# Optimization experiments

Measured on AMD Instinct MI355X. Metric: run time of the kernel, lower is better.

## Reference

```python
import jax, jax.numpy as jnp
import numpy as np

B, L, D, H = 4, 1024, 768, 12
HD = D // H  # head_dim = 64
SCALING = HD ** -0.5


def setup_inputs() -> dict:
    key = jax.random.key(0)
    ks = jax.random.split(key, 6)
    x = jax.random.normal(ks[0], (B, L, D), dtype=jnp.float32)
    attn_bias = jax.random.normal(ks[1], (B, H, L, L), dtype=jnp.float32)
    s_in = 1.0 / np.sqrt(D)
    w_in = jax.random.uniform(ks[2], (3 * D, D), dtype=jnp.float32, minval=-s_in, maxval=s_in)
    b_in = jax.random.uniform(ks[3], (3 * D,), dtype=jnp.float32, minval=-s_in, maxval=s_in)
    w_out = jax.random.uniform(ks[4], (D, D), dtype=jnp.float32, minval=-s_in, maxval=s_in)
    b_out = jax.random.uniform(ks[5], (D,), dtype=jnp.float32, minval=-s_in, maxval=s_in)
    return {"x": x, "attn_bias": attn_bias, "w_in": w_in, "b_in": b_in,
            "w_out": w_out, "b_out": b_out}


def reference(x, attn_bias, w_in, b_in, w_out, b_out):
    # fused QKV projection: [B, L, 3D]
    qkv = jnp.einsum('bld,ed->ble', x, w_in) + b_in
    q, k, v = jnp.split(qkv, 3, axis=-1)
    # [B, H, L, HD]
    q = q.reshape(B, L, H, HD).transpose(0, 2, 1, 3) * SCALING
    k = k.reshape(B, L, H, HD).transpose(0, 2, 1, 3)
    v = v.reshape(B, L, H, HD).transpose(0, 2, 1, 3)
    # bias-augmented attention scores: [B, H, L, L]
    scores = jnp.einsum('bhqd,bhkd->bhqk', q, k) + attn_bias
    probs = jax.nn.softmax(scores, axis=-1)
    # attend: [B, H, L, HD] -> [B, L, D]
    o = jnp.einsum('bhqk,bhkd->bhqd', probs, v)
    o = o.transpose(0, 2, 1, 3).reshape(B, L, D)
    return jnp.einsum('bld,ed->ble', o, w_out) + b_out
```

## Files before the change

kernel.cpp:

```cpp
#include <hip/hip_runtime.h>
#include <hip/hip_bf16.h>
#include <stdint.h>

#define B_ 4
#define L_ 1024
#define D_ 768
#define H_ 12
#define HD_ 64
#define M_ 4096
#define N3_ 2304

typedef float f32x4 __attribute__((ext_vector_type(4)));
typedef float f32x4v __attribute__((ext_vector_type(4)));
typedef short bf16x8 __attribute__((ext_vector_type(8)));
typedef unsigned short u16;
typedef u16 u16x8 __attribute__((ext_vector_type(8)));
typedef u16 u16x4 __attribute__((ext_vector_type(4)));

#define AS3 __attribute__((address_space(3)))
#define AS1 __attribute__((address_space(1)))

__device__ __forceinline__ void gll16(const void* g, void* l) {
  __builtin_amdgcn_global_load_lds((const AS1 void*)g, (AS3 void*)l, 16, 0, 0);
}

__device__ __forceinline__ u16 f2bf(float f) {
  uint32_t u = __builtin_bit_cast(uint32_t, f);
  u += 0x7fffu + ((u >> 16) & 1u);
  return (u16)(u >> 16);
}

__global__ void k_cvt(const float* __restrict__ in, u16* __restrict__ out, int n4) {
  int i = blockIdx.x * 256 + threadIdx.x;
  if (i < n4) {
    f32x4v v = ((const f32x4v*)in)[i];
    u16x4 o;
    o.x = f2bf(v.x); o.y = f2bf(v.y); o.z = f2bf(v.z); o.w = f2bf(v.w);
    ((u16x4*)out)[i] = o;
  }
}

__global__ __launch_bounds__(256) void k_gemm_qkv(
    const u16* __restrict__ Xb, const u16* __restrict__ Wb,
    const float* __restrict__ b_in,
    u16* __restrict__ gQ, u16* __restrict__ gK, u16* __restrict__ gV) {
  __shared__ u16 As[128 * 64];
  __shared__ u16 Bs[128 * 64];
  const int tid = threadIdx.x;
  const int lane = tid & 63;
  const int w = tid >> 6;
  const int wm = (w >> 1) * 64;
  const int wn = (w & 1) * 64;
  const int lr = lane & 15;
  const int lg = lane >> 4;
  const int m0 = blockIdx.x * 128;
  const int n0 = blockIdx.y * 128;

  f32x4 acc[4][4];
#pragma unroll
  for (int i = 0; i < 4; ++i)
#pragma unroll
    for (int j = 0; j < 4; ++j) acc[i][j] = (f32x4){0.f, 0.f, 0.f, 0.f};

  for (int kt = 0; kt < 12; ++kt) {
    __syncthreads();
#pragma unroll
    for (int i = 0; i < 4; ++i) {
      int seg = i * 256 + tid;
      int row = seg >> 3;
      int sl = (seg & 7) ^ (row & 7);
      gll16(Xb + (size_t)(m0 + row) * 768 + kt * 64 + sl * 8, (char*)As + seg * 16);
      gll16(Wb + (size_t)(n0 + row) * 768 + kt * 64 + sl * 8, (char*)Bs + seg * 16);
    }
    __syncthreads();
#pragma unroll
    for (int kh = 0; kh < 2; ++kh) {
      bf16x8 af[4], bfr[4];
#pragma unroll
      for (int t = 0; t < 4; ++t) {
        int ra = wm + t * 16 + lr;
        af[t] = *(const bf16x8*)((const char*)As + ra * 128 +
                                 ((kh * 64 + lg * 16) ^ ((ra & 7) << 4)));
        int rb = wn + t * 16 + lr;
        bfr[t] = *(const bf16x8*)((const char*)Bs + rb * 128 +
                                  ((kh * 64 + lg * 16) ^ ((rb & 7) << 4)));
      }
#pragma unroll
      for (int mi = 0; mi < 4; ++mi)
#pragma unroll
        for (int ni = 0; ni < 4; ++ni)
          acc[mi][ni] = __builtin_amdgcn_mfma_f32_16x16x32_bf16(
              af[mi], bfr[ni], acc[mi][ni], 0, 0, 0);
    }
  }
  const int sec = blockIdx.y / 6;
  u16* dst = sec == 0 ? gQ : (sec == 1 ? gK : gV);
  const float scale = sec == 0 ? 0.125f : 1.0f;
#pragma unroll
  for (int ni = 0; ni < 4; ++ni) {
    int e = n0 + wn + ni * 16 + lr;
    float bias = b_in[e];
    int es = e - sec * 768;
    int h = es >> 6, d = es & 63;
#pragma unroll
    for (int mi = 0; mi < 4; ++mi) {
#pragma unroll
      for (int j = 0; j < 4; ++j) {
        int m = m0 + wm + mi * 16 + lg * 4 + j;
        int bb = m >> 10, lq = m & 1023;
        float vv = (acc[mi][ni][j] + bias) * scale;
        dst[(size_t)((bb * 12 + h) * 1024 + lq) * 64 + d] = f2bf(vv);
      }
    }
  }
}

__global__ __launch_bounds__(256) void k_transpose(const u16* __restrict__ V,
                                                   u16* __restrict__ Vt) {
  __shared__ u16 t[64][66];
  const int tid = threadIdx.x;
  const int bh = blockIdx.x >> 4;
  const int kv0 = (blockIdx.x & 15) * 64;
  {
    int r = tid >> 2, c0 = (tid & 3) * 16;
    const u16* src = V + (size_t)(bh * 1024 + kv0 + r) * 64 + c0;
#pragma unroll
    for (int p = 0; p < 2; ++p) {
      u16x8 x = *(const u16x8*)(src + p * 8);
#pragma unroll
      for (int e = 0; e < 8; ++e) t[r][c0 + p * 8 + e] = x[e];
    }
  }
  __syncthreads();
  {
    int d = tid >> 2, k0 = (tid & 3) * 16;
    u16* dst = Vt + (size_t)(bh * 64 + d) * 1024 + kv0 + k0;
#pragma unroll
    for (int p = 0; p < 2; ++p) {
      u16x8 o;
#pragma unroll
      for (int e = 0; e < 8; ++e) o[e] = t[k0 + p * 8 + e][d];
      *(u16x8*)(dst + p * 8) = o;
    }
  }
}

__global__ __launch_bounds__(256) void k_attn(
    const u16* __restrict__ gQ, const u16* __restrict__ gK,
    const u16* __restrict__ gVt, const float* __restrict__ gBias,
    u16* __restrict__ gO) {
  __shared__ u16 Ks[64 * 64];
  __shared__ u16 Vs[64 * 64];
  __shared__ u16 Pl[4][16 * 64];
  const int tid = threadIdx.x;
  const int lane = tid & 63;
  const int w = tid >> 6;
  const int lr = lane & 15;
  const int lg = lane >> 4;
  const int bh = blockIdx.x >> 4;
  const int q0 = (blockIdx.x & 15) * 64;
  const int qr = q0 + w * 16;

  bf16x8 qa[2];
#pragma unroll
  for (int kh = 0; kh < 2; ++kh)
    qa[kh] = *(const bf16x8*)(gQ + (size_t)(bh * 1024 + qr + lr) * 64 + kh * 32 + lg * 8);

  f32x4 oacc[4];
#pragma unroll
  for (int dt = 0; dt < 4; ++dt) oacc[dt] = (f32x4){0.f, 0.f, 0.f, 0.f};
  float mrow[4] = {-1e30f, -1e30f, -1e30f, -1e30f};
  float lrow[4] = {0.f, 0.f, 0.f, 0.f};

  for (int kv0 = 0; kv0 < 1024; kv0 += 64) {
    __syncthreads();
#pragma unroll
    for (int i = 0; i < 2; ++i) {
      int seg = i * 256 + tid;
      int row = seg >> 3;
      int sl = (seg & 7) ^ (row & 7);
      gll16(gK + (size_t)(bh * 1024 + kv0 + row) * 64 + sl * 8, (char*)Ks + seg * 16);
      gll16(gVt + (size_t)(bh * 64 + row) * 1024 + kv0 + sl * 8, (char*)Vs + seg * 16);
    }
    __syncthreads();

    f32x4 s[4];
#pragma unroll
    for (int ni = 0; ni < 4; ++ni) s[ni] = (f32x4){0.f, 0.f, 0.f, 0.f};
#pragma unroll
    for (int kh = 0; kh < 2; ++kh) {
#pragma unroll
      for (int ni = 0; ni < 4; ++ni) {
        int rb = ni * 16 + lr;
        bf16x8 kb = *(const bf16x8*)((const char*)Ks + rb * 128 +
                                     ((kh * 64 + lg * 16) ^ ((rb & 7) << 4)));
        s[ni] = __builtin_amdgcn_mfma_f32_16x16x32_bf16(qa[kh], kb, s[ni], 0, 0, 0);
      }
    }
    const float* bp = gBias + (size_t)(bh * 1024 + qr) * 1024 + kv0;
#pragma unroll
    for (int ni = 0; ni < 4; ++ni)
#pragma unroll
      for (int j = 0; j < 4; ++j)
        s[ni][j] += bp[(size_t)(lg * 4 + j) * 1024 + ni * 16 + lr];

#pragma unroll
    for (int j = 0; j < 4; ++j) {
      float vm = fmaxf(fmaxf(s[0][j], s[1][j]), fmaxf(s[2][j], s[3][j]));
      vm = fmaxf(vm, __shfl_xor(vm, 1));
      vm = fmaxf(vm, __shfl_xor(vm, 2));
      vm = fmaxf(vm, __shfl_xor(vm, 4));
      vm = fmaxf(vm, __shfl_xor(vm, 8));
      float mnew = fmaxf(mrow[j], vm);
      float al = __expf(mrow[j] - mnew);
      mrow[j] = mnew;
      float rs = 0.f;
#pragma unroll
      for (int ni = 0; ni < 4; ++ni) {
        float p = __expf(s[ni][j] - mnew);
        s[ni][j] = p;
        rs += p;
      }
      rs += __shfl_xor(rs, 1);
      rs += __shfl_xor(rs, 2);
      rs += __shfl_xor(rs, 4);
      rs += __shfl_xor(rs, 8);
      lrow[j] = lrow[j] * al + rs;
#pragma unroll
      for (int dt = 0; dt < 4; ++dt) oacc[dt][j] *= al;
    }

    u16* pw = Pl[w];
#pragma unroll
    for (int ni = 0; ni < 4; ++ni)
#pragma unroll
      for (int j = 0; j < 4; ++j) {
        int row = lg * 4 + j;
        int bc = (ni * 16 + lr) * 2;
        *(u16*)((char*)pw + row * 128 + (bc ^ ((row & 7) << 4))) = f2bf(s[ni][j]);
      }
#pragma unroll
    for (int kh = 0; kh < 2; ++kh) {
      bf16x8 pa = *(const bf16x8*)((const char*)pw + lr * 128 +
                                   ((kh * 64 + lg * 16) ^ ((lr & 7) << 4)));
#pragma unroll
      for (int dt = 0; dt < 4; ++dt) {
        int rv = dt * 16 + lr;
        bf16x8 vb = *(const bf16x8*)((const char*)Vs + rv * 128 +
                                     ((kh * 64 + lg * 16) ^ ((rv & 7) << 4)));
        oacc[dt] = __builtin_amdgcn_mfma_f32_16x16x32_bf16(pa, vb, oacc[dt], 0, 0, 0);
      }
    }
  }

  const int bg = bh / 12, h = bh % 12;
#pragma unroll
  for (int j = 0; j < 4; ++j) {
    float inv = 1.0f / lrow[j];
    int row = qr + lg * 4 + j;
#pragma unroll
    for (int dt = 0; dt < 4; ++dt) {
      gO[(size_t)(bg * 1024 + row) * 768 + h * 64 + dt * 16 + lr] =
          f2bf(oacc[dt][j] * inv);
    }
  }
}

__global__ __launch_bounds__(256) void k_gemm_out(
    const u16* __restrict__ Ob, const u16* __restrict__ Wb,
    const float* __restrict__ b_out, float* __restrict__ out) {
  __shared__ u16 As[128 * 64];
  __shared__ u16 Bs[128 * 64];
  const int tid = threadIdx.x;
  const int lane = tid & 63;
  const int w = tid >> 6;
  const int wm = (w >> 1) * 64;
  const int wn = (w & 1) * 64;
  const int lr = lane & 15;
  const int lg = lane >> 4;
  const int m0 = blockIdx.x * 128;
  const int n0 = blockIdx.y * 128;

  f32x4 acc[4][4];
#pragma unroll
  for (int i = 0; i < 4; ++i)
#pragma unroll
    for (int j = 0; j < 4; ++j) acc[i][j] = (f32x4){0.f, 0.f, 0.f, 0.f};

  for (int kt = 0; kt < 12; ++kt) {
    __syncthreads();
#pragma unroll
    for (int i = 0; i < 4; ++i) {
      int seg = i * 256 + tid;
      int row = seg >> 3;
      int sl = (seg & 7) ^ (row & 7);
      gll16(Ob + (size_t)(m0 + row) * 768 + kt * 64 + sl * 8, (char*)As + seg * 16);
      gll16(Wb + (size_t)(n0 + row) * 768 + kt * 64 + sl * 8, (char*)Bs + seg * 16);
    }
    __syncthreads();
#pragma unroll
    for (int kh = 0; kh < 2; ++kh) {
      bf16x8 af[4], bfr[4];
#pragma unroll
      for (int t = 0; t < 4; ++t) {
        int ra = wm + t * 16 + lr;
        af[t] = *(const bf16x8*)((const char*)As + ra * 128 +
                                 ((kh * 64 + lg * 16) ^ ((ra & 7) << 4)));
        int rb = wn + t * 16 + lr;
        bfr[t] = *(const bf16x8*)((const char*)Bs + rb * 128 +
                                  ((kh * 64 + lg * 16) ^ ((rb & 7) << 4)));
      }
#pragma unroll
      for (int mi = 0; mi < 4; ++mi)
#pragma unroll
        for (int ni = 0; ni < 4; ++ni)
          acc[mi][ni] = __builtin_amdgcn_mfma_f32_16x16x32_bf16(
              af[mi], bfr[ni], acc[mi][ni], 0, 0, 0);
    }
  }
#pragma unroll
  for (int ni = 0; ni < 4; ++ni) {
    int n = n0 + wn + ni * 16 + lr;
    float bias = b_out[n];
#pragma unroll
    for (int mi = 0; mi < 4; ++mi) {
#pragma unroll
      for (int j = 0; j < 4; ++j) {
        int m = m0 + wm + mi * 16 + lg * 4 + j;
        out[(size_t)m * 768 + n] = acc[mi][ni][j] + bias;
      }
    }
  }
}

extern "C" void kernel_launch(void* const* d_in, const int* in_sizes, int n_in,
                              void* d_out, int out_size, void* d_ws, size_t ws_size,
                              hipStream_t stream) {
  const float* x = (const float*)d_in[0];
  const float* attn_bias = (const float*)d_in[1];
  const float* w_in = (const float*)d_in[2];
  const float* b_in = (const float*)d_in[3];
  const float* w_out = (const float*)d_in[4];
  const float* b_out = (const float*)d_in[5];
  float* out = (float*)d_out;

  char* ws = (char*)d_ws;
  size_t off = 0;
  u16* xb = (u16*)(ws + off);  off += (size_t)M_ * D_ * 2;
  u16* wib = (u16*)(ws + off); off += (size_t)N3_ * D_ * 2;
  u16* wob = (u16*)(ws + off); off += (size_t)D_ * D_ * 2;
  u16* q = (u16*)(ws + off);   off += (size_t)48 * 1024 * 64 * 2;
  u16* k = (u16*)(ws + off);   off += (size_t)48 * 1024 * 64 * 2;
  u16* v = (u16*)(ws + off);   off += (size_t)48 * 1024 * 64 * 2;
  u16* vt = (u16*)(ws + off);  off += (size_t)48 * 1024 * 64 * 2;
  u16* ob = (u16*)(ws + off);  off += (size_t)M_ * D_ * 2;

  k_cvt<<<3072, 256, 0, stream>>>(x, xb, (M_ * D_) / 4);
  k_cvt<<<1728, 256, 0, stream>>>(w_in, wib, (N3_ * D_) / 4);
  k_cvt<<<576, 256, 0, stream>>>(w_out, wob, (D_ * D_) / 4);
  k_gemm_qkv<<<dim3(32, 18), 256, 0, stream>>>(xb, wib, b_in, q, k, v);
  k_transpose<<<768, 256, 0, stream>>>(v, vt);
  k_attn<<<768, 256, 0, stream>>>(q, k, vt, attn_bias, ob);
  k_gemm_out<<<dim3(32, 6), 256, 0, stream>>>(ob, wob, b_out, out);
}
```

Measured before the change: 124.1 us.

## Double-buffer K/V tiles and prefetch bias in attention, fuse conversion kernels

The attention kernel now double-buffers K and V tiles in LDS and issues the next tile's async global-to-LDS loads before computing on the current one. It also prefetches the next tile's bias values into registers with nontemporal loads, raises wave priority around the MFMA blocks, and remaps block indices across XCDs. The three fp32-to-bf16 conversion launches are merged into one kernel. The aim is to hide global latency behind compute and cut launch overhead, at the cost of doubled LDS use and extra registers, which may lower occupancy.

```diff
diff --git a/kernel.cpp b/kernel.cpp
--- a/kernel.cpp
+++ b/kernel.cpp
@@ -30,14 +30,25 @@
   return (u16)(u >> 16);
 }
 
-__global__ void k_cvt(const float* __restrict__ in, u16* __restrict__ out, int n4) {
+__global__ void k_cvt3(const float* __restrict__ a, u16* __restrict__ ao, int na4,
+                       const float* __restrict__ b, u16* __restrict__ bo, int nb4,
+                       const float* __restrict__ c, u16* __restrict__ co, int nc4) {
   int i = blockIdx.x * 256 + threadIdx.x;
-  if (i < n4) {
-    f32x4v v = ((const f32x4v*)in)[i];
-    u16x4 o;
-    o.x = f2bf(v.x); o.y = f2bf(v.y); o.z = f2bf(v.z); o.w = f2bf(v.w);
-    ((u16x4*)out)[i] = o;
-  }
+  const float* src;
+  u16* dst;
+  if (i < na4) {
+    src = a; dst = ao;
+  } else if (i < na4 + nb4) {
+    src = b; dst = bo; i -= na4;
+  } else if (i < na4 + nb4 + nc4) {
+    src = c; dst = co; i -= na4 + nb4;
+  } else {
+    return;
+  }
+  f32x4v v = ((const f32x4v*)src)[i];
+  u16x4 o;
+  o.x = f2bf(v.x); o.y = f2bf(v.y); o.z = f2bf(v.z); o.w = f2bf(v.w);
+  ((u16x4*)dst)[i] = o;
 }
 
 __global__ __launch_bounds__(256) void k_gemm_qkv(
@@ -149,17 +160,31 @@
     const u16* __restrict__ gQ, const u16* __restrict__ gK,
     const u16* __restrict__ gVt, const float* __restrict__ gBias,
     u16* __restrict__ gO) {
-  __shared__ u16 Ks[64 * 64];
-  __shared__ u16 Vs[64 * 64];
+  __shared__ u16 Ks[2][64 * 64];
+  __shared__ u16 Vs[2][64 * 64];
   __shared__ u16 Pl[4][16 * 64];
   const int tid = threadIdx.x;
   const int lane = tid & 63;
   const int w = tid >> 6;
   const int lr = lane & 15;
   const int lg = lane >> 4;
-  const int bh = blockIdx.x >> 4;
-  const int q0 = (blockIdx.x & 15) * 64;
+  const int lb = (blockIdx.x & 7) * 96 + (blockIdx.x >> 3);
+  const int bh = lb >> 4;
+  const int q0 = (lb & 15) * 64;
   const int qr = q0 + w * 16;
+
+#define STAGE_KV(buf, kv0)                                                         \
+  do {                                                                             \
+    _Pragma("unroll") for (int i_ = 0; i_ < 2; ++i_) {                             \
+      int seg_ = i_ * 256 + tid;                                                   \
+      int row_ = seg_ >> 3;                                                        \
+      int sl_ = (seg_ & 7) ^ (row_ & 7);                                           \
+      gll16(gK + (size_t)(bh * 1024 + (kv0) + row_) * 64 + sl_ * 8,                \
+            (char*)Ks[buf] + seg_ * 16);                                           \
+      gll16(gVt + (size_t)(bh * 64 + row_) * 1024 + (kv0) + sl_ * 8,               \
+            (char*)Vs[buf] + seg_ * 16);                                           \
+    }                                                                              \
+  } while (0)
 
   bf16x8 qa[2];
 #pragma unroll
@@ -172,37 +197,53 @@
   float mrow[4] = {-1e30f, -1e30f, -1e30f, -1e30f};
   float lrow[4] = {0.f, 0.f, 0.f, 0.f};
 
-  for (int kv0 = 0; kv0 < 1024; kv0 += 64) {
-    __syncthreads();
-#pragma unroll
-    for (int i = 0; i < 2; ++i) {
-      int seg = i * 256 + tid;
-      int row = seg >> 3;
-      int sl = (seg & 7) ^ (row & 7);
-      gll16(gK + (size_t)(bh * 1024 + kv0 + row) * 64 + sl * 8, (char*)Ks + seg * 16);
-      gll16(gVt + (size_t)(bh * 64 + row) * 1024 + kv0 + sl * 8, (char*)Vs + seg * 16);
-    }
-    __syncthreads();
+  const float* bbase = gBias + (size_t)(bh * 1024 + qr) * 1024;
+
+  STAGE_KV(0, 0);
+  float bcur[16];
+#pragma unroll
+  for (int ni = 0; ni < 4; ++ni)
+#pragma unroll
+    for (int j = 0; j < 4; ++j)
+      bcur[ni * 4 + j] = __builtin_nontemporal_load(
+          bbase + (size_t)(lg * 4 + j) * 1024 + ni * 16 + lr);
+  __syncthreads();
+
+  for (int t = 0; t < 16; ++t) {
+    const int cur = t & 1;
+    if (t < 15) STAGE_KV(cur ^ 1, (t + 1) * 64);
 
     f32x4 s[4];
 #pragma unroll
     for (int ni = 0; ni < 4; ++ni) s[ni] = (f32x4){0.f, 0.f, 0.f, 0.f};
+    __builtin_amdgcn_s_setprio(1);
 #pragma unroll
     for (int kh = 0; kh < 2; ++kh) {
 #pragma unroll
       for (int ni = 0; ni < 4; ++ni) {
         int rb = ni * 16 + lr;
-        bf16x8 kb = *(const bf16x8*)((const char*)Ks + rb * 128 +
+        bf16x8 kb = *(const bf16x8*)((const char*)Ks[cur] + rb * 128 +
                                      ((kh * 64 + lg * 16) ^ ((rb & 7) << 4)));
         s[ni] = __builtin_amdgcn_mfma_f32_16x16x32_bf16(qa[kh], kb, s[ni], 0, 0, 0);
       }
     }
-    const float* bp = gBias + (size_t)(bh * 1024 + qr) * 1024 + kv0;
+    __builtin_amdgcn_s_setprio(0);
+
 #pragma unroll
     for (int ni = 0; ni < 4; ++ni)
 #pragma unroll
-      for (int j = 0; j < 4; ++j)
-        s[ni][j] += bp[(size_t)(lg * 4 + j) * 1024 + ni * 16 + lr];
+      for (int j = 0; j < 4; ++j) s[ni][j] += bcur[ni * 4 + j];
+
+    float bnx[16];
+    if (t < 15) {
+      const float* bp = bbase + (t + 1) * 64;
+#pragma unroll
+      for (int ni = 0; ni < 4; ++ni)
+#pragma unroll
+        for (int j = 0; j < 4; ++j)
+          bnx[ni * 4 + j] = __builtin_nontemporal_load(
+              bp + (size_t)(lg * 4 + j) * 1024 + ni * 16 + lr);
+    }
 
 #pragma unroll
     for (int j = 0; j < 4; ++j) {
@@ -239,6 +280,7 @@
         int bc = (ni * 16 + lr) * 2;
         *(u16*)((char*)pw + row * 128 + (bc ^ ((row & 7) << 4))) = f2bf(s[ni][j]);
       }
+    __builtin_amdgcn_s_setprio(1);
 #pragma unroll
     for (int kh = 0; kh < 2; ++kh) {
       bf16x8 pa = *(const bf16x8*)((const char*)pw + lr * 128 +
@@ -246,11 +288,18 @@
 #pragma unroll
       for (int dt = 0; dt < 4; ++dt) {
         int rv = dt * 16 + lr;
-        bf16x8 vb = *(const bf16x8*)((const char*)Vs + rv * 128 +
+        bf16x8 vb = *(const bf16x8*)((const char*)Vs[cur] + rv * 128 +
                                      ((kh * 64 + lg * 16) ^ ((rv & 7) << 4)));
         oacc[dt] = __builtin_amdgcn_mfma_f32_16x16x32_bf16(pa, vb, oacc[dt], 0, 0, 0);
       }
     }
+    __builtin_amdgcn_s_setprio(0);
+
+    if (t < 15) {
+#pragma unroll
+      for (int z = 0; z < 16; ++z) bcur[z] = bnx[z];
+    }
+    __syncthreads();
   }
 
   const int bg = bh / 12, h = bh % 12;
@@ -264,6 +313,7 @@
           f2bf(oacc[dt][j] * inv);
     }
   }
+#undef STAGE_KV
 }
 
 __global__ __launch_bounds__(256) void k_gemm_out(
@@ -355,9 +405,11 @@
   u16* vt = (u16*)(ws + off);  off += (size_t)48 * 1024 * 64 * 2;
   u16* ob = (u16*)(ws + off);  off += (size_t)M_ * D_ * 2;
 
-  k_cvt<<<3072, 256, 0, stream>>>(x, xb, (M_ * D_) / 4);
-  k_cvt<<<1728, 256, 0, stream>>>(w_in, wib, (N3_ * D_) / 4);
-  k_cvt<<<576, 256, 0, stream>>>(w_out, wob, (D_ * D_) / 4);
+  const int na4 = (M_ * D_) / 4;
+  const int nb4 = (N3_ * D_) / 4;
+  const int nc4 = (D_ * D_) / 4;
+  k_cvt3<<<(na4 + nb4 + nc4 + 255) / 256, 256, 0, stream>>>(
+      x, xb, na4, w_in, wib, nb4, w_out, wob, nc4);
   k_gemm_qkv<<<dim3(32, 18), 256, 0, stream>>>(xb, wib, b_in, q, k, v);
   k_transpose<<<768, 256, 0, stream>>>(v, vt);
   k_attn<<<768, 256, 0, stream>>>(q, k, vt, attn_bias, ob);
```

After: 130.0 us. 1.05x slower.
